# Optimization experiments

Hardware: AMD Instinct MI355X
Metric: run time of the kernel (lower is better)

Reference implementation:

```python
import jax, jax.numpy as jnp
import numpy as np

A, C, H, W = 8, 256, 80, 108      # agents, channels, cf_h, cf_w from the module
NUM_CLASSES = 7
OUT_H, OUT_W = 256, 256


def warp_affine(feat, M):
    """Bilinear affine warp of feat [C,H,W] with sampling matrix M [2,3].
    dst(u,v) = src(M @ [u,v,1]); out-of-bounds samples are zero (kornia zero padding)."""
    c, h, w = feat.shape
    vs, us = jnp.meshgrid(jnp.arange(h, dtype=feat.dtype),
                          jnp.arange(w, dtype=feat.dtype), indexing='ij')
    sx = M[0, 0] * us + M[0, 1] * vs + M[0, 2]
    sy = M[1, 0] * us + M[1, 1] * vs + M[1, 2]
    x0 = jnp.floor(sx)
    y0 = jnp.floor(sy)
    wx = sx - x0
    wy = sy - y0
    x0i = x0.astype(jnp.int32)
    y0i = y0.astype(jnp.int32)

    def tap(yy, xx, wgt):
        valid = (yy >= 0) & (yy < h) & (xx >= 0) & (xx < w)
        yyc = jnp.clip(yy, 0, h - 1)
        xxc = jnp.clip(xx, 0, w - 1)
        return feat[:, yyc, xxc] * (wgt * valid)[None]

    return (tap(y0i, x0i, (1 - wy) * (1 - wx))
            + tap(y0i, x0i + 1, (1 - wy) * wx)
            + tap(y0i + 1, x0i, wy * (1 - wx))
            + tap(y0i + 1, x0i + 1, wy * wx))


def resize_bilinear_align_corners(img, oh, ow):
    """F.interpolate(..., mode='bilinear', align_corners=True) for img [N,C,H,W]."""
    h, w = img.shape[-2:]
    ys = jnp.linspace(0.0, h - 1.0, oh, dtype=img.dtype)
    xs = jnp.linspace(0.0, w - 1.0, ow, dtype=img.dtype)
    y0 = jnp.clip(jnp.floor(ys).astype(jnp.int32), 0, h - 2)
    x0 = jnp.clip(jnp.floor(xs).astype(jnp.int32), 0, w - 2)
    wy = (ys - y0)[None, None, :, None]
    wx = (xs - x0)[None, None, None, :]
    row = img[:, :, y0, :] * (1 - wy) + img[:, :, y0 + 1, :] * wy   # [N,C,oh,W]
    return row[:, :, :, x0] * (1 - wx) + row[:, :, :, x0 + 1] * wx  # [N,C,oh,ow]


def setup_inputs() -> dict:
    key = jax.random.key(0)
    k1, k2, k3, k4, k5, k6 = jax.random.split(key, 6)
    x = jax.random.normal(k1, (A, C, H, W), jnp.float32)
    # near-identity per-pair affine sampling matrices with small rotation/shear + translation
    rel = jnp.tile(jnp.eye(2, 3, dtype=jnp.float32), (A, A, 1, 1))
    rel = rel + 0.05 * jax.random.normal(k2, (A, A, 2, 3), jnp.float32)
    rel = rel.at[..., 2].add(10.0 * jax.random.normal(k3, (A, A, 2), jnp.float32))
    adjacency_matrix = jax.random.randint(k4, (A, A), 0, 2, dtype=jnp.int32)
    car_masks = jax.random.uniform(k5, (A, 256, 256), jnp.float32)
    w_cls = 0.02 * jax.random.normal(k6, (NUM_CLASSES, C), jnp.float32)
    b_cls = jnp.zeros((NUM_CLASSES,), jnp.float32)
    return {"x": x, "relative_tfs": rel, "adjacency_matrix": adjacency_matrix,
            "car_masks": car_masks, "w_cls": w_cls, "b_cls": b_cls}


def reference(x, relative_tfs, adjacency_matrix, car_masks, w_cls, b_cls):
    # x = x + F.interpolate(car_masks.unsqueeze(1), (cf_h, cf_w), 'bilinear')  (align_corners=False)
    cm = jax.image.resize(car_masks[:, None], (A, 1, H, W), method="bilinear")
    x = x + cm

    # aggregate_features: per ego-agent i, warp all agents' features into i's frame,
    # zero agents with adjacency[i,j]==0, and sum over j.
    warp_all = jax.vmap(warp_affine)                       # over agents j
    warped = jax.vmap(lambda Ms: warp_all(x, Ms))(relative_tfs)  # [A,A,C,H,W]
    fov = (adjacency_matrix != 0).astype(x.dtype)          # [A,A]
    aggr = jnp.einsum('ij,ijchw->ichw', fov, warped)       # masked sum over j

    def predict(f):  # mask_prediction (1x1 conv) + sigmoid
        logits = jnp.einsum('oc,achw->aohw', w_cls, f) + b_cls[None, :, None, None]
        return jax.nn.sigmoid(logits)

    solo_x = resize_bilinear_align_corners(predict(x), OUT_H, OUT_W)
    aggr_x = resize_bilinear_align_corners(predict(aggr), OUT_H, OUT_W)
    return (solo_x, aggr_x)
```

## Files before the change

kernel.cpp:

```cpp
#include <hip/hip_runtime.h>
#include <hip/hip_bf16.h>

#define A_N 8
#define C_N 256
#define H_N 80
#define W_N 108
#define P_N (H_N * W_N)
#define O_N 7
#define MH 256
#define MW 256
#define OUT_HW 256

#define TILE   512
#define NTIL   17
#define GSP    2
#define CPG2   (C_N / GSP)

__device__ __forceinline__ float sigmoidf_(float zv) {
    return 1.0f / (1.0f + __expf(-zv));
}

__launch_bounds__(512)
__global__ void k_convp(const float* __restrict__ x, const float* __restrict__ w,
                        float* __restrict__ part)
{
    const int bi   = blockIdx.x;
    const int g    = bi & 1;
    const int t2   = bi >> 1;
    const int tile = t2 % NTIL;
    const int a    = t2 / NTIL;

    const int px  = tile * TILE + threadIdx.x;
    const int pxc = min(px, P_N - 1);

    float acc[O_N];
    #pragma unroll
    for (int o = 0; o < O_N; ++o) acc[o] = 0.0f;

    const float* xp = x + ((size_t)a * C_N + g * CPG2) * P_N + pxc;
    const float* wp = w + g * CPG2;

    #pragma unroll 8
    for (int cc = 0; cc < CPG2; ++cc) {
        float v = xp[(size_t)cc * P_N];
        #pragma unroll
        for (int o = 0; o < O_N; ++o)
            acc[o] = fmaf(wp[o * C_N + cc], v, acc[o]);
    }

    if (px < P_N) {
        const size_t pb = ((size_t)(g * A_N + a) * O_N) * P_N + px;
        #pragma unroll
        for (int o = 0; o < O_N; ++o)
            part[pb + (size_t)o * P_N] = acc[o];
    }
}

__launch_bounds__(256)
__global__ void k_finalize(const float* __restrict__ part, const float* __restrict__ masks,
                           const float* __restrict__ w, const float* __restrict__ b,
                           float* __restrict__ z, float* __restrict__ ssolo)
{
    __shared__ float s_wsum[O_N];
    if (threadIdx.x < O_N) {
        const float4* wr = reinterpret_cast<const float4*>(w + threadIdx.x * C_N);
        float s = 0.0f;
        #pragma unroll 4
        for (int c4 = 0; c4 < C_N / 4; ++c4) { float4 v = wr[c4]; s += v.x + v.y + v.z + v.w; }
        s_wsum[threadIdx.x] = s;
    }
    __syncthreads();

    const int idx = blockIdx.x * 256 + threadIdx.x;
    const int a = idx / P_N, p = idx - a * P_N;
    const int oy = p / W_N, ox = p - oy * W_N;

    const float ksy = 256.0f / 80.0f;
    const float ksx = 256.0f / 108.0f;
    const float rky = 0.3125f;
    const float rkx = 0.421875f;

    float sfy = ((float)oy + 0.5f) * ksy - 0.5f;
    float sfx = ((float)ox + 0.5f) * ksx - 0.5f;
    int iy0 = max(0, (int)ceilf(sfy - ksy));
    int iy1 = min(MH - 1, (int)floorf(sfy + ksy));
    int ix0 = max(0, (int)ceilf(sfx - ksx));
    int ix1 = min(MW - 1, (int)floorf(sfx + ksx));

    float wys = 0.0f, wxs = 0.0f;
    for (int iy = iy0; iy <= iy1; ++iy)
        wys += fmaxf(0.0f, 1.0f - fabsf(sfy - (float)iy) * rky);
    for (int ix = ix0; ix <= ix1; ++ix)
        wxs += fmaxf(0.0f, 1.0f - fabsf(sfx - (float)ix) * rkx);

    const float* mp = masks + a * (MH * MW);
    float acc = 0.0f;
    for (int iy = iy0; iy <= iy1; ++iy) {
        float wyv = fmaxf(0.0f, 1.0f - fabsf(sfy - (float)iy) * rky);
        const float* row = mp + iy * MW;
        float racc = 0.0f;
        for (int ix = ix0; ix <= ix1; ++ix)
            racc += fmaxf(0.0f, 1.0f - fabsf(sfx - (float)ix) * rkx) * row[ix];
        acc += wyv * racc;
    }
    const float cmv = acc / (wys * wxs);

    const size_t p0 = ((size_t)(0 * A_N + a) * O_N) * P_N + p;
    const size_t p1 = ((size_t)(1 * A_N + a) * O_N) * P_N + p;
    const size_t zb = ((size_t)a * O_N) * P_N + p;
    #pragma unroll
    for (int o = 0; o < O_N; ++o) {
        float zv = part[p0 + (size_t)o * P_N] + part[p1 + (size_t)o * P_N]
                 + s_wsum[o] * cmv;
        z[zb + (size_t)o * P_N]     = zv;
        ssolo[zb + (size_t)o * P_N] = sigmoidf_(zv + b[o]);
    }
}

__launch_bounds__(64)
__global__ void k_aggr(const float* __restrict__ z, const float* __restrict__ rel,
                       const int* __restrict__ adj, const float* __restrict__ b,
                       float* __restrict__ saggr)
{
    const int i = blockIdx.x / 135;
    const int p = (blockIdx.x - i * 135) * 64 + threadIdx.x;
    const int vy = p / W_N, ux = p - vy * W_N;
    const float fu = (float)ux, fv = (float)vy;

    float acc[O_N];
    #pragma unroll
    for (int o = 0; o < O_N; ++o) acc[o] = b[o];

    for (int j = 0; j < A_N; ++j) {
        if (adj[i * A_N + j] == 0) continue;
        const float* M = rel + (i * A_N + j) * 6;
        float sx = M[0] * fu + M[1] * fv + M[2];
        float sy = M[3] * fu + M[4] * fv + M[5];
        if (!(sx > -1.0f && sx < (float)W_N && sy > -1.0f && sy < (float)H_N)) continue;
        float x0f = floorf(sx), y0f = floorf(sy);
        float wx = sx - x0f, wy = sy - y0f;
        int x0 = (int)x0f, y0 = (int)y0f;
        int x1 = x0 + 1,  y1 = y0 + 1;
        float w00 = (1.0f - wy) * (1.0f - wx), w01 = (1.0f - wy) * wx;
        float w10 = wy * (1.0f - wx),          w11 = wy * wx;
        if (x0 < 0)    { w00 = 0.0f; w10 = 0.0f; x0 = 0; }
        if (x1 >= W_N) { w01 = 0.0f; w11 = 0.0f; x1 = W_N - 1; }
        if (y0 < 0)    { w00 = 0.0f; w01 = 0.0f; y0 = 0; }
        if (y1 >= H_N) { w10 = 0.0f; w11 = 0.0f; y1 = H_N - 1; }
        const int i00 = y0 * W_N + x0, i01 = y0 * W_N + x1;
        const int i10 = y1 * W_N + x0, i11 = y1 * W_N + x1;
        const float* zj = z + j * O_N * P_N;
        #pragma unroll
        for (int o = 0; o < O_N; ++o) {
            const float* zp = zj + o * P_N;
            acc[o] += w00 * zp[i00] + w01 * zp[i01] + w10 * zp[i10] + w11 * zp[i11];
        }
    }
    const int ob = i * O_N * P_N + p;
    #pragma unroll
    for (int o = 0; o < O_N; ++o) saggr[ob + o * P_N] = sigmoidf_(acc[o]);
}

__launch_bounds__(256)
__global__ void k_upsample(const float* __restrict__ ssolo, const float* __restrict__ saggr,
                           float* __restrict__ out)
{
    const int idx = blockIdx.x * 256 + threadIdx.x;
    int k = idx;
    const int oxq = k & 63;   k >>= 6;
    const int oy  = k & 255;  k >>= 8;
    const int o   = k % O_N;  k /= O_N;
    const int a   = k & 7;    k >>= 3;
    const int t   = k;

    const float* src = (t == 0 ? ssolo : saggr) + (a * O_N + o) * P_N;
    float syf = (float)oy * (79.0f / 255.0f);
    int y0 = (int)syf; y0 = min(y0, H_N - 2);
    float wy = syf - (float)y0;
    const float* r0 = src + y0 * W_N;
    const float* r1 = r0 + W_N;

    float res[4];
    #pragma unroll
    for (int q = 0; q < 4; ++q) {
        int ox = oxq * 4 + q;
        float sxf = (float)ox * (107.0f / 255.0f);
        int x0 = (int)sxf; x0 = min(x0, W_N - 2);
        float wx = sxf - (float)x0;
        float c0 = r0[x0]     * (1.0f - wy) + r1[x0]     * wy;
        float c1 = r0[x0 + 1] * (1.0f - wy) + r1[x0 + 1] * wy;
        res[q] = c0 * (1.0f - wx) + c1 * wx;
    }
    *reinterpret_cast<float4*>(out + (size_t)idx * 4) =
        make_float4(res[0], res[1], res[2], res[3]);
}

extern "C" void kernel_launch(void* const* d_in, const int* in_sizes, int n_in,
                              void* d_out, int out_size, void* d_ws, size_t ws_size,
                              hipStream_t stream)
{
    (void)in_sizes; (void)n_in; (void)out_size; (void)ws_size;
    const float* x    = (const float*)d_in[0];
    const float* rel  = (const float*)d_in[1];
    const int*   adj  = (const int*)d_in[2];
    const float* cmsk = (const float*)d_in[3];
    const float* wcls = (const float*)d_in[4];
    const float* bcls = (const float*)d_in[5];
    float* out = (float*)d_out;

    float* ws    = (float*)d_ws;
    float* part  = ws;
    float* z     = part  + GSP * A_N * O_N * P_N;
    float* ssolo = z     + A_N * O_N * P_N;
    float* saggr = ssolo + A_N * O_N * P_N;

    k_convp   <<<A_N * NTIL * GSP, TILE, 0, stream>>>(x, wcls, part);
    k_finalize<<<270, 256, 0, stream>>>(part, cmsk, wcls, bcls, z, ssolo);
    k_aggr    <<<1080, 64, 0, stream>>>(z, rel, adj, bcls, saggr);
    k_upsample<<<7168, 256, 0, stream>>>(ssolo, saggr, out);
}
```

Before: 48.13 us.

## Vectorize conv partials with float4 pixels, 4-way channel split, unroll mask resize

The 1x1 conv kernel now has each thread handle four adjacent pixels with float4 loads, so each weight load is reused four times. Channels are split into four groups instead of two, and the grid shrinks to 270 blocks of 256 threads. The mask-resize taps in finalize are now fixed-size unrolled loops with clamped indices and zeroed out-of-range weights, and finalize sums four partials. Fewer threads and more registers per thread may lower occupancy and latency hiding in the bandwidth-bound conv.

```diff
diff --git a/kernel.cpp b/kernel.cpp
--- a/kernel.cpp
+++ b/kernel.cpp
@@ -6,54 +6,53 @@
 #define H_N 80
 #define W_N 108
 #define P_N (H_N * W_N)
+#define P4_N (P_N / 4)
 #define O_N 7
 #define MH 256
 #define MW 256
 #define OUT_HW 256
 
-#define TILE   512
-#define NTIL   17
-#define GSP    2
-#define CPG2   (C_N / GSP)
+#define GSP  4
+#define CPG  (C_N / GSP)
 
 __device__ __forceinline__ float sigmoidf_(float zv) {
     return 1.0f / (1.0f + __expf(-zv));
 }
 
-__launch_bounds__(512)
+__launch_bounds__(256)
 __global__ void k_convp(const float* __restrict__ x, const float* __restrict__ w,
                         float* __restrict__ part)
 {
-    const int bi   = blockIdx.x;
-    const int g    = bi & 1;
-    const int t2   = bi >> 1;
-    const int tile = t2 % NTIL;
-    const int a    = t2 / NTIL;
-
-    const int px  = tile * TILE + threadIdx.x;
-    const int pxc = min(px, P_N - 1);
-
-    float acc[O_N];
-    #pragma unroll
-    for (int o = 0; o < O_N; ++o) acc[o] = 0.0f;
-
-    const float* xp = x + ((size_t)a * C_N + g * CPG2) * P_N + pxc;
-    const float* wp = w + g * CPG2;
+    const int i   = blockIdx.x * 256 + threadIdx.x;
+    const int px4 = i % P4_N;
+    const int ag  = i / P4_N;
+    const int a   = ag >> 2;
+    const int g   = ag & 3;
+
+    float4 acc[O_N];
+    #pragma unroll
+    for (int o = 0; o < O_N; ++o) acc[o] = make_float4(0.f, 0.f, 0.f, 0.f);
+
+    const float4* xp = reinterpret_cast<const float4*>(x)
+                     + (size_t)(a * C_N + g * CPG) * P4_N + px4;
+    const float*  wp = w + g * CPG;
 
     #pragma unroll 8
-    for (int cc = 0; cc < CPG2; ++cc) {
-        float v = xp[(size_t)cc * P_N];
-        #pragma unroll
-        for (int o = 0; o < O_N; ++o)
-            acc[o] = fmaf(wp[o * C_N + cc], v, acc[o]);
-    }
-
-    if (px < P_N) {
-        const size_t pb = ((size_t)(g * A_N + a) * O_N) * P_N + px;
-        #pragma unroll
-        for (int o = 0; o < O_N; ++o)
-            part[pb + (size_t)o * P_N] = acc[o];
-    }
+    for (int cc = 0; cc < CPG; ++cc) {
+        float4 v = xp[(size_t)cc * P4_N];
+        #pragma unroll
+        for (int o = 0; o < O_N; ++o) {
+            float wv = wp[o * C_N + cc];
+            acc[o].x = fmaf(wv, v.x, acc[o].x);
+            acc[o].y = fmaf(wv, v.y, acc[o].y);
+            acc[o].z = fmaf(wv, v.z, acc[o].z);
+            acc[o].w = fmaf(wv, v.w, acc[o].w);
+        }
+    }
+
+    float4* pp = reinterpret_cast<float4*>(part) + (size_t)(ag * O_N) * P4_N + px4;
+    #pragma unroll
+    for (int o = 0; o < O_N; ++o) pp[(size_t)o * P4_N] = acc[o];
 }
 
 __launch_bounds__(256)
@@ -80,40 +79,48 @@
     const float rky = 0.3125f;
     const float rkx = 0.421875f;
 
-    float sfy = ((float)oy + 0.5f) * ksy - 0.5f;
-    float sfx = ((float)ox + 0.5f) * ksx - 0.5f;
-    int iy0 = max(0, (int)ceilf(sfy - ksy));
-    int iy1 = min(MH - 1, (int)floorf(sfy + ksy));
-    int ix0 = max(0, (int)ceilf(sfx - ksx));
-    int ix1 = min(MW - 1, (int)floorf(sfx + ksx));
-
-    float wys = 0.0f, wxs = 0.0f;
-    for (int iy = iy0; iy <= iy1; ++iy)
-        wys += fmaxf(0.0f, 1.0f - fabsf(sfy - (float)iy) * rky);
-    for (int ix = ix0; ix <= ix1; ++ix)
-        wxs += fmaxf(0.0f, 1.0f - fabsf(sfx - (float)ix) * rkx);
-
-    const float* mp = masks + a * (MH * MW);
-    float acc = 0.0f;
-    for (int iy = iy0; iy <= iy1; ++iy) {
-        float wyv = fmaxf(0.0f, 1.0f - fabsf(sfy - (float)iy) * rky);
-        const float* row = mp + iy * MW;
-        float racc = 0.0f;
-        for (int ix = ix0; ix <= ix1; ++ix)
-            racc += fmaxf(0.0f, 1.0f - fabsf(sfx - (float)ix) * rkx) * row[ix];
-        acc += wyv * racc;
+    const float sfy = ((float)oy + 0.5f) * ksy - 0.5f;
+    const float sfx = ((float)ox + 0.5f) * ksx - 0.5f;
+    const int iyS = (int)ceilf(sfy - ksy);
+    const int ixS = (int)ceilf(sfx - ksx);
+
+    float wxv[5];
+    float wxs = 0.0f;
+    #pragma unroll
+    for (int q = 0; q < 5; ++q) {
+        const int ix = ixS + q;
+        float wv = fmaxf(0.0f, 1.0f - fabsf(sfx - (float)ix) * rkx);
+        wv = (ix >= 0 && ix < MW) ? wv : 0.0f;
+        wxv[q] = wv;
+        wxs += wv;
+    }
+
+    const float* mp = masks + (size_t)a * (MH * MW);
+    float acc = 0.0f, wys = 0.0f;
+    #pragma unroll
+    for (int r = 0; r < 7; ++r) {
+        const int iy = iyS + r;
+        float wy = fmaxf(0.0f, 1.0f - fabsf(sfy - (float)iy) * rky);
+        wy = (iy >= 0 && iy < MH) ? wy : 0.0f;
+        wys += wy;
+        const float* row = mp + min(max(iy, 0), MH - 1) * MW;
+        float rs = 0.0f;
+        #pragma unroll
+        for (int q = 0; q < 5; ++q)
+            rs = fmaf(wxv[q], row[min(max(ixS + q, 0), MW - 1)], rs);
+        acc = fmaf(wy, rs, acc);
     }
     const float cmv = acc / (wys * wxs);
 
-    const size_t p0 = ((size_t)(0 * A_N + a) * O_N) * P_N + p;
-    const size_t p1 = ((size_t)(1 * A_N + a) * O_N) * P_N + p;
-    const size_t zb = ((size_t)a * O_N) * P_N + p;
     #pragma unroll
     for (int o = 0; o < O_N; ++o) {
-        float zv = part[p0 + (size_t)o * P_N] + part[p1 + (size_t)o * P_N]
-                 + s_wsum[o] * cmv;
-        z[zb + (size_t)o * P_N]     = zv;
-        ssolo[zb + (size_t)o * P_N] = sigmoidf_(zv + b[o]);
+        float s = 0.0f;
+        #pragma unroll
+        for (int g = 0; g < GSP; ++g)
+            s += part[(size_t)((a * GSP + g) * O_N + o) * P_N + p];
+        const float zv = s + s_wsum[o] * cmv;
+        z[(size_t)(a * O_N + o) * P_N + p]     = zv;
+        ssolo[(size_t)(a * O_N + o) * P_N + p] = sigmoidf_(zv + b[o]);
     }
 }
 
@@ -214,7 +221,7 @@
     float* ssolo = z     + A_N * O_N * P_N;
     float* saggr = ssolo + A_N * O_N * P_N;
 
-    k_convp   <<<A_N * NTIL * GSP, TILE, 0, stream>>>(x, wcls, part);
+    k_convp   <<<270, 256, 0, stream>>>(x, wcls, part);
     k_finalize<<<270, 256, 0, stream>>>(part, cmsk, wcls, bcls, z, ssolo);
     k_aggr    <<<1080, 64, 0, stream>>>(z, rel, adj, bcls, saggr);
     k_upsample<<<7168, 256, 0, stream>>>(ssolo, saggr, out);
```

Result: slower. 53.36 us (+10.9%).
